# Kernel tuning notes

Hardware: AMD Instinct MI355X
Metric: run time of the kernel (lower is better)

Reference implementation:

```python
import jax, jax.numpy as jnp
import numpy as np

B, S, D_IN, D_OUT, L = 16, 1024, 768, 768, 2
ALPHA = 0.2  # LeakyReLU negative slope
NEG_INF = -1e12


def setup_inputs() -> dict:
    key = jax.random.key(0)
    ks = jax.random.split(key, 6)
    input_feature = jax.random.normal(ks[0], (B, S, D_IN), dtype=jnp.float32)
    matrix = jax.random.randint(ks[1], (B, S, S), 0, 2, dtype=jnp.int32)
    # per-layer params (stacked along leading L axis)
    sw = 1.0 / np.sqrt(D_IN)
    W = jax.random.uniform(ks[2], (L, D_OUT, D_IN), jnp.float32, -sw, sw)
    Wb = jax.random.uniform(ks[3], (L, D_OUT), jnp.float32, -sw, sw)
    sa = 1.0 / np.sqrt(2 * D_OUT)
    A = jax.random.uniform(ks[4], (L, 2 * D_OUT), jnp.float32, -sa, sa)
    Ab = jax.random.uniform(ks[5], (L,), jnp.float32, -sa, sa)
    return {"input_feature": input_feature, "matrix": matrix,
            "W": W, "Wb": Wb, "A": A, "Ab": Ab}


def reference(input_feature, matrix, W, Wb, A, Ab):
    # Eval mode: dropout(p=0.1, training=False) is identity.
    hidden = input_feature
    mask = matrix > 0  # [B,S,S]
    outs = []
    for l in range(L):
        h = jnp.einsum('bsd,od->bso', hidden, W[l]) + Wb[l]  # [B,S,Dout]
        # a([h_i, h_j]) == h_i @ a_src + h_j @ a_dst + b  (exact separation)
        a_src, a_dst = A[l, :D_OUT], A[l, D_OUT:]
        s_i = h @ a_src  # [B,S]
        s_j = h @ a_dst  # [B,S]
        e = jax.nn.leaky_relu(s_i[:, :, None] + s_j[:, None, :] + Ab[l], ALPHA)
        e = jnp.where(mask, e, NEG_INF)
        attn = jax.nn.softmax(e, axis=1)  # original softmaxes over dim=1
        hidden = jnp.einsum('bij,bjd->bid', attn, h)
        outs.append(hidden)
    return jnp.stack(outs)  # [L,B,S,Dout]
```

## Files before the change

### kernel.cpp

```cpp
#include <hip/hip_runtime.h>
#include <cstddef>

#define SS 1024
#define DF 768
#define NBATCH 16
#define GAT_ALPHA 0.2f

typedef _Float16 f16x8 __attribute__((ext_vector_type(8)));
typedef _Float16 f16x4 __attribute__((ext_vector_type(4)));
typedef float f32x4 __attribute__((ext_vector_type(4)));

__device__ __forceinline__ void gload16(const void* g, void* l) {
  __builtin_amdgcn_global_load_lds(
      (const __attribute__((address_space(1))) void*)g,
      (__attribute__((address_space(3))) void*)l, 16, 0, 0);
}

__device__ __forceinline__ float lrelu(float t) {
  return fmaxf(t, GAT_ALPHA * t);
}

__global__ __launch_bounds__(256) void f32tof16_k(const float* __restrict__ in,
                                                  _Float16* __restrict__ out,
                                                  int n) {
  int idx = (blockIdx.x * 256 + threadIdx.x) * 4;
  if (idx + 3 < n) {
    float4 v = *(const float4*)&in[idx];
    f16x4 o;
    o[0] = (_Float16)v.x;
    o[1] = (_Float16)v.y;
    o[2] = (_Float16)v.z;
    o[3] = (_Float16)v.w;
    *(f16x4*)&out[idx] = o;
  }
}

__global__ __launch_bounds__(256) void pack_k(const int* __restrict__ mask,
                                              unsigned char* __restrict__ bm) {
  const size_t t = (size_t)blockIdx.x * 256 + threadIdx.x;
  const int* mp = mask + t * 8;
  const int4 a = *(const int4*)mp;
  const int4 c = *(const int4*)(mp + 4);
  unsigned v = (unsigned)(a.x > 0) | ((unsigned)(a.y > 0) << 1) |
               ((unsigned)(a.z > 0) << 2) | ((unsigned)(a.w > 0) << 3) |
               ((unsigned)(c.x > 0) << 4) | ((unsigned)(c.y > 0) << 5) |
               ((unsigned)(c.z > 0) << 6) | ((unsigned)(c.w > 0) << 7);
  bm[t] = (unsigned char)v;
}

__global__ __launch_bounds__(512, 2) void gemm1_k(
    const _Float16* __restrict__ X16, const _Float16* __restrict__ W16,
    const float* __restrict__ Wbl, const float* __restrict__ Al,
    _Float16* __restrict__ hT16, float* __restrict__ psi2,
    float* __restrict__ psj2) {
  __shared__ __align__(16) char smem[131072];
  const int flat = blockIdx.x;
  const int swz = (flat & 7) * 32 + (flat >> 3);
  const int m0 = (swz >> 1) * 128;
  const int n0 = (swz & 1) * 384;
  const int tid = threadIdx.x;
  const int w = tid >> 6, lane = tid & 63;

  const int srow = w * 16 + (lane >> 2);
  const int sk8 = ((lane & 3) ^ ((lane >> 3) & 3)) * 8;
  const int rby = ((lane >> 4) ^ ((lane >> 1) & 3)) * 16;
  const int rrow = lane & 15;

  f32x4 acc[8][3];
#pragma unroll
  for (int mi = 0; mi < 8; ++mi)
#pragma unroll
    for (int ni = 0; ni < 3; ++ni) acc[mi][ni] = (f32x4)(0.f);

#define STGA1(s, kt)                                                       \
  gload16(&X16[(size_t)(m0 + srow) * DF + (kt) * 32 + sk8],                \
          smem + (s) * 32768 + w * 1024)
#define STGB1(s, kt, q)                                                    \
  gload16(&W16[(size_t)(n0 + (q) * 128 + srow) * DF + (kt) * 32 + sk8],    \
          smem + (s) * 32768 + 8192 + (q) * 8192 + w * 1024)

  const int NT = DF / 32;
  STGA1(0, 0); STGB1(0, 0, 0); STGB1(0, 0, 1); STGB1(0, 0, 2);
  STGA1(1, 1); STGB1(1, 1, 0); STGB1(1, 1, 1); STGB1(1, 1, 2);
  asm volatile("s_waitcnt vmcnt(4)" ::: "memory");
  asm volatile("s_barrier" ::: "memory");

  for (int t = 0; t < NT; ++t) {
    const int s = t & 3;
    const char* Ab = smem + s * 32768;
    const char* Bb = smem + s * 32768 + 8192;
    f16x8 bfr[3], afr[8];
#pragma unroll
    for (int ni = 0; ni < 3; ++ni)
      bfr[ni] = *(const f16x8*)(Bb + (w * 48 + ni * 16 + rrow) * 64 + rby);
#pragma unroll
    for (int mi = 0; mi < 8; ++mi)
      afr[mi] = *(const f16x8*)(Ab + (mi * 16 + rrow) * 64 + rby);
    if (t + 2 < NT) {
      const int s2 = (t + 2) & 3;
      STGA1(s2, t + 2);
      STGB1(s2, t + 2, 0);
      STGB1(s2, t + 2, 1);
      STGB1(s2, t + 2, 2);
    }
    if (t < NT - 2)
      asm volatile("s_waitcnt vmcnt(4)" ::: "memory");
    else
      asm volatile("s_waitcnt vmcnt(0)" ::: "memory");
    asm volatile("s_barrier" ::: "memory");
    __builtin_amdgcn_s_setprio(1);
#pragma unroll
    for (int mi = 0; mi < 8; ++mi)
#pragma unroll
      for (int ni = 0; ni < 3; ++ni)
        acc[mi][ni] = __builtin_amdgcn_mfma_f32_16x16x32_f16(
            afr[mi], bfr[ni], acc[mi][ni], 0, 0, 0);
    __builtin_amdgcn_s_setprio(0);
  }
#undef STGA1
#undef STGB1

  __syncthreads();
  _Float16* tb = (_Float16*)smem + (size_t)w * 6528;
  float* asrc = (float*)(smem + 104448);
  float* adst = asrc + 384;
  float* pwsi = adst + 384;
  float* pwsj = pwsi + 1024;

  for (int i = tid; i < 384; i += 512) {
    asrc[i] = Al[n0 + i];
    adst[i] = Al[DF + n0 + i];
  }
  const int cg = lane >> 4, cr = lane & 15;
  float bias[3];
#pragma unroll
  for (int ni = 0; ni < 3; ++ni) bias[ni] = Wbl[n0 + w * 48 + ni * 16 + cr];
#pragma unroll
  for (int mi = 0; mi < 8; ++mi) {
#pragma unroll
    for (int ni = 0; ni < 3; ++ni) {
      f16x4 tv;
#pragma unroll
      for (int r = 0; r < 4; ++r)
        tv[r] = (_Float16)(acc[mi][ni][r] + bias[ni]);
      *(f16x4*)&tb[(ni * 16 + cr) * 136 + mi * 16 + cg * 4] = tv;
    }
  }
  __syncthreads();

  const float* wa = asrc + w * 48;
  const float* wdp = adst + w * 48;
#pragma unroll
  for (int rr = 0; rr < 2; ++rr) {
    const int r = lane + rr * 64;
    float ps = 0.f, pd = 0.f;
#pragma unroll 8
    for (int c = 0; c < 48; ++c) {
      const float hv = (float)tb[c * 136 + r];
      ps = fmaf(hv, wa[c], ps);
      pd = fmaf(hv, wdp[c], pd);
    }
    pwsi[w * 128 + r] = ps;
    pwsj[w * 128 + r] = pd;
  }
  __syncthreads();
  if (tid < 128) {
    float s = 0.f, d2 = 0.f;
#pragma unroll
    for (int ww = 0; ww < 8; ++ww) {
      s += pwsi[ww * 128 + tid];
      d2 += pwsj[ww * 128 + tid];
    }
    const int nt = swz & 1;
    psi2[nt * 16384 + m0 + tid] = s;
    psj2[nt * 16384 + m0 + tid] = d2;
  }

  const int bb = m0 >> 10, s0 = m0 & 1023;
#pragma unroll
  for (int pass = 0; pass < 12; ++pass) {
    const int c = pass * 4 + (lane >> 4);
    f16x8 v = *(const f16x8*)&tb[c * 136 + (lane & 15) * 8];
    *(f16x8*)&hT16[((size_t)bb * DF + n0 + w * 48 + c) * SS + s0 +
                   (lane & 15) * 8] = v;
  }
}

__global__ __launch_bounds__(512, 2) void gemm2_k(
    const unsigned char* __restrict__ bmk, const float* __restrict__ si_g,
    const unsigned int* __restrict__ sq_g, const _Float16* __restrict__ hT16,
    float* __restrict__ outl, _Float16* __restrict__ X16n, int writeX) {
  __shared__ __align__(16) char smem[153600];
  const int flat = blockIdx.x;
  const int swz = (flat & 7) * 32 + (flat >> 3);
  const int b = swz >> 4;
  const int i0 = ((swz >> 1) & 7) * 128;
  const int d0 = (swz & 1) * 384;
  const int tid = threadIdx.x;
  const int w = tid >> 6, lane = tid & 63;

  const int srow = w * 16 + (lane >> 2);
  const int sk8 = ((lane & 3) ^ ((lane >> 3) & 3)) * 8;
  const int rby = ((lane >> 4) ^ ((lane >> 1) & 3)) * 16;
  const int rrow = lane & 15;

  const int pr = tid >> 2, pc = tid & 3;
  const int ppos = pc ^ ((pr >> 1) & 3);

  const _Float16* hTb = hT16 + (size_t)b * DF * SS;

  f32x4 acc[8][3];
#pragma unroll
  for (int mi = 0; mi < 8; ++mi)
#pragma unroll
    for (int ni = 0; ni < 3; ++ni) acc[mi][ni] = (f32x4)(0.f);

#define STGB2(s, kt, q)                                                    \
  gload16(&hTb[((size_t)(d0 + (q) * 128 + srow)) * SS + (kt) * 32 + sk8],  \
          smem + (s) * 32768 + 8192 + (q) * 8192 + w * 1024)

#define COMPUTE_P(kt, slot)                                                  \
  {                                                                          \
    const unsigned mw =                                                      \
        *(const unsigned*)(smem + 135168 + pr * 144 + (kt) * 4);             \
    const unsigned mb = (mw >> (pc * 8)) & 0xffu;                            \
    const f16x8 sA_ =                                                        \
        *(const f16x8*)(smem + 131072 + (kt) * 128 + pc * 32);               \
    const f16x8 sB_ =                                                        \
        *(const f16x8*)(smem + 131072 + (kt) * 128 + pc * 32 + 16);          \
    f16x8 ph;                                                                \
    _Pragma("unroll") for (int jj = 0; jj < 4; ++jj) {                       \
      const float sjcv = (float)sA_[2 * jj];                                 \
      const float qv = (float)sA_[2 * jj + 1];                               \
      const float ttv = siv + sjcv;                                          \
      const float ev = __expf(fmaxf(ttv, 0.2f * ttv)) * qv;                  \
      ph[jj] = (_Float16)(qv < 0.f ? -qv : (((mb >> jj) & 1u) ? ev : 0.f));  \
    }                                                                        \
    _Pragma("unroll") for (int jj = 0; jj < 4; ++jj) {                       \
      const float sjcv = (float)sB_[2 * jj];                                 \
      const float qv = (float)sB_[2 * jj + 1];                               \
      const float ttv = siv + sjcv;                                          \
      const float ev = __expf(fmaxf(ttv, 0.2f * ttv)) * qv;                  \
      ph[4 + jj] = (_Float16)(qv < 0.f ? -qv                                 \
                                       : (((mb >> (4 + jj)) & 1u) ? ev       \
                                                                  : 0.f));   \
    }                                                                        \
    *(f16x8*)(smem + (slot) * 32768 + pr * 64 + ppos * 16) = ph;             \
  }

  const unsigned char* bmb = bmk + ((size_t)b << 17) + ((size_t)i0 << 7);
  const uint4 mg0 = *(const uint4*)(bmb + tid * 32);
  const uint4 mg1 = *(const uint4*)(bmb + tid * 32 + 16);
  if (w < 4)
    gload16(&sq_g[(b << 10) + w * 256 + lane * 4], smem + 131072 + w * 1024);
  const float siv = si_g[(b << 10) + i0 + pr];
  const int NT = SS / 32;
  STGB2(0, 0, 0); STGB2(0, 0, 1); STGB2(0, 0, 2);
  STGB2(1, 1, 0); STGB2(1, 1, 1); STGB2(1, 1, 2);
  asm volatile("s_waitcnt vmcnt(0)" ::: "memory");
  *(uint4*)(smem + 135168 + pr * 144 + pc * 32) = mg0;
  *(uint4*)(smem + 135168 + pr * 144 + pc * 32 + 16) = mg1;
  asm volatile("s_waitcnt lgkmcnt(0)" ::: "memory");
  asm volatile("s_barrier" ::: "memory");
  COMPUTE_P(0, 0);
  asm volatile("s_waitcnt lgkmcnt(0)" ::: "memory");
  asm volatile("s_barrier" ::: "memory");

  for (int t = 0; t < NT; ++t) {
    const char* Ab = smem + (t & 3) * 32768;
    const char* Bb = Ab + 8192;
    f16x8 bfr[3], afr[8];
#pragma unroll
    for (int ni = 0; ni < 3; ++ni)
      bfr[ni] = *(const f16x8*)(Bb + (w * 48 + ni * 16 + rrow) * 64 + rby);
#pragma unroll
    for (int mi = 0; mi < 8; ++mi)
      afr[mi] = *(const f16x8*)(Ab + (mi * 16 + rrow) * 64 + rby);
    if (t + 1 < NT) COMPUTE_P(t + 1, (t + 1) & 3);
    if (t + 2 < NT) {
      const int s2 = (t + 2) & 3;
      STGB2(s2, t + 2, 0);
      STGB2(s2, t + 2, 1);
      STGB2(s2, t + 2, 2);
    }
    if (t < NT - 2)
      asm volatile("s_waitcnt vmcnt(3) lgkmcnt(0)" ::: "memory");
    else
      asm volatile("s_waitcnt vmcnt(0) lgkmcnt(0)" ::: "memory");
    asm volatile("s_barrier" ::: "memory");
    __builtin_amdgcn_s_setprio(1);
#pragma unroll
    for (int mi = 0; mi < 8; ++mi)
#pragma unroll
      for (int ni = 0; ni < 3; ++ni)
        acc[mi][ni] = __builtin_amdgcn_mfma_f32_16x16x32_f16(
            afr[mi], bfr[ni], acc[mi][ni], 0, 0, 0);
    __builtin_amdgcn_s_setprio(0);
  }
#undef STGB2
#undef COMPUTE_P

  const int cg = lane >> 4, cr = lane & 15;
#pragma unroll
  for (int mi = 0; mi < 8; ++mi) {
#pragma unroll
    for (int ni = 0; ni < 3; ++ni) {
      const int d = d0 + w * 48 + ni * 16 + cr;
      const int row0 = i0 + mi * 16 + cg * 4;
#pragma unroll
      for (int r = 0; r < 4; ++r) {
        float v = acc[mi][ni][r];
        size_t o = ((size_t)b * SS + row0 + r) * DF + d;
        outl[o] = v;
        if (writeX) X16n[o] = (_Float16)v;
      }
    }
  }
}

__global__ __launch_bounds__(256) void rowfin_k(const float* __restrict__ psi2,
                                                const float* __restrict__ psj2,
                                                const float* __restrict__ Abp,
                                                float* __restrict__ si,
                                                float* __restrict__ sjc,
                                                float* __restrict__ refj) {
  const int b = blockIdx.x;
  const int t = threadIdx.x;
  __shared__ float red[256];
  float siv[4], sjv[4];
  float mloc = -1e30f;
#pragma unroll
  for (int q = 0; q < 4; ++q) {
    const int idx = (b << 10) + t + (q << 8);
    const float a = psi2[idx] + psi2[16384 + idx];
    const float d = psj2[idx] + psj2[16384 + idx];
    siv[q] = a;
    sjv[q] = d;
    si[idx] = a;
    mloc = fmaxf(mloc, a);
  }
  red[t] = mloc;
  __syncthreads();
  for (int off = 128; off > 0; off >>= 1) {
    if (t < off) red[t] = fmaxf(red[t], red[t + off]);
    __syncthreads();
  }
  const float maxsi = red[0];
  const float ab = Abp[0];
#pragma unroll
  for (int q = 0; q < 4; ++q) {
    const int idx = (b << 10) + t + (q << 8);
    const float c = sjv[q] + ab;
    sjc[idx] = c;
    refj[idx] = lrelu(maxsi + c);
  }
}

__global__ __launch_bounds__(256) void colsum_k(
    const unsigned char* __restrict__ bm, const float* __restrict__ si,
    const float* __restrict__ sjc, const float* __restrict__ refj,
    float* __restrict__ pden) {
  const int g = blockIdx.x;
  const int b = blockIdx.y;
  const int t = threadIdx.x;
  const int jb = t & 127;
  const int half = t >> 7;
  const int row0 = (g << 5) + (half << 4);
  __shared__ float s_si[32];
  if (t < 32) s_si[t] = si[(b << 10) + (g << 5) + t];
  __syncthreads();
  float sc[8], rf[8];
  *(float4*)&sc[0] = *(const float4*)&sjc[(b << 10) + jb * 8];
  *(float4*)&sc[4] = *(const float4*)&sjc[(b << 10) + jb * 8 + 4];
  *(float4*)&rf[0] = *(const float4*)&refj[(b << 10) + jb * 8];
  *(float4*)&rf[4] = *(const float4*)&refj[(b << 10) + jb * 8 + 4];
  float den[8] = {0.f, 0.f, 0.f, 0.f, 0.f, 0.f, 0.f, 0.f};
  const unsigned char* bp = bm + ((size_t)b << 17) + ((size_t)row0 << 7) + jb;
#pragma unroll 4
  for (int r = 0; r < 16; ++r) {
    const unsigned m = bp[(size_t)r << 7];
    const float siv = s_si[(half << 4) + r];
#pragma unroll
    for (int k = 0; k < 8; ++k) {
      if ((m >> k) & 1) den[k] += __expf(lrelu(siv + sc[k]) - rf[k]);
    }
  }
  const size_t o = ((size_t)(g * 2 + half)) * 16384 + (b << 10) + jb * 8;
  *(float4*)&pden[o] = *(float4*)&den[0];
  *(float4*)&pden[o + 4] = *(float4*)&den[4];
}

__global__ __launch_bounds__(256) void colfin_k(const float* __restrict__ pden,
                                                const float* __restrict__ sjc,
                                                const float* __restrict__ refj,
                                                unsigned int* __restrict__ sq) {
  const int idx = blockIdx.x * 256 + threadIdx.x;
  float s = 0.f;
#pragma unroll
  for (int c = 0; c < 64; ++c) s += pden[(size_t)c * 16384 + idx];
  const float q = (s > 0.f) ? __expf(-refj[idx]) / s : -0.0009765625f;
  const _Float16 h0 = (_Float16)sjc[idx];
  const _Float16 h1 = (_Float16)q;
  unsigned short u0, u1;
  __builtin_memcpy(&u0, &h0, 2);
  __builtin_memcpy(&u1, &h1, 2);
  sq[idx] = ((unsigned)u1 << 16) | (unsigned)u0;
}

extern "C" void kernel_launch(void* const* d_in, const int* in_sizes, int n_in,
                              void* d_out, int out_size, void* d_ws,
                              size_t ws_size, hipStream_t stream) {
  const float* X0 = (const float*)d_in[0];
  const int* mask = (const int*)d_in[1];
  const float* W = (const float*)d_in[2];
  const float* Wb = (const float*)d_in[3];
  const float* A = (const float*)d_in[4];
  const float* Ab = (const float*)d_in[5];
  float* out = (float*)d_out;

  const size_t BSD = (size_t)NBATCH * SS * DF;
  const size_t BSS = (size_t)NBATCH * SS * SS;
  const size_t BS = (size_t)NBATCH * SS;

  char* p = (char*)d_ws;
  _Float16* X16 = (_Float16*)p;   p += BSD * 2;
  _Float16* hT16 = (_Float16*)p;  p += BSD * 2;
  _Float16* W16 = (_Float16*)p;   p += (size_t)2 * DF * DF * 2;
  unsigned char* bmk = (unsigned char*)p; p += BSS / 8;
  float* psi2 = (float*)p; p += 2 * BS * 4;
  float* psj2 = (float*)p; p += 2 * BS * 4;
  float* pden = (float*)p; p += 64 * BS * 4;
  float* si = (float*)p;   p += BS * 4;
  float* sjc = (float*)p;  p += BS * 4;
  float* refj = (float*)p; p += BS * 4;
  unsigned int* sq_g = (unsigned int*)p; p += BS * 4;

  f32tof16_k<<<12288, 256, 0, stream>>>(X0, X16, (int)BSD);
  f32tof16_k<<<1152, 256, 0, stream>>>(W, W16, 2 * DF * DF);
  pack_k<<<8192, 256, 0, stream>>>(mask, bmk);

  for (int l = 0; l < 2; ++l) {
    gemm1_k<<<256, 512, 0, stream>>>(X16, W16 + (size_t)l * DF * DF,
                                     Wb + (size_t)l * DF,
                                     A + (size_t)l * 2 * DF, hT16, psi2, psj2);
    rowfin_k<<<16, 256, 0, stream>>>(psi2, psj2, Ab + l, si, sjc, refj);
    colsum_k<<<dim3(32, 16), 256, 0, stream>>>(bmk, si, sjc, refj, pden);
    colfin_k<<<64, 256, 0, stream>>>(pden, sjc, refj, sq_g);
    gemm2_k<<<256, 512, 0, stream>>>(bmk, si, sq_g, hT16,
                                     out + (size_t)l * BSD, X16,
                                     (l == 0) ? 1 : 0);
  }
}
```

Measured before the change: 246.2 us.

## Factor LeakyReLU exponentials into per-row and per-column terms, removing exp from inner loops

Uses exp(lrelu(si+sj)) = exp(si)exp(sj) or exp(0.2si)exp(0.2sj), depending on the sign of si+sj. Per-row exponentials are computed once, and per-column scale factors are precomputed in colfin. colsum then accumulates two partial sums without any exp calls. gemm2's P computation becomes an fp16 select and multiply instead of an exp per element. The cost is double the partial-sum buffers and sq traffic, and a risk of fp16 overflow or precision loss in the factored products (e.g. exp(si) in half).

```diff
diff --git a/kernel.cpp b/kernel.cpp
--- a/kernel.cpp
+++ b/kernel.cpp
@@ -188,9 +188,9 @@
 
 __global__ __launch_bounds__(512, 2) void gemm2_k(
     const unsigned char* __restrict__ bmk, const float* __restrict__ si_g,
-    const unsigned int* __restrict__ sq_g, const _Float16* __restrict__ hT16,
+    const uint2* __restrict__ sq_g, const _Float16* __restrict__ hT16,
     float* __restrict__ outl, _Float16* __restrict__ X16n, int writeX) {
-  __shared__ __align__(16) char smem[153600];
+  __shared__ __align__(16) char smem[157696];
   const int flat = blockIdx.x;
   const int swz = (flat & 7) * 32 + (flat >> 3);
   const int b = swz >> 4;
@@ -219,47 +219,51 @@
   gload16(&hTb[((size_t)(d0 + (q) * 128 + srow)) * SS + (kt) * 32 + sk8],  \
           smem + (s) * 32768 + 8192 + (q) * 8192 + w * 1024)
 
+#define PCALC(sjch, c1h, c2h, mbit)                                        \
+  ((c2h) < (_Float16)0.f                                                   \
+       ? (_Float16)0.0009765625f                                           \
+       : (!(mbit) ? (_Float16)0.f                                          \
+                  : ((_Float16)(sih + (sjch)) >= (_Float16)0.f             \
+                         ? (_Float16)(e1h * (c1h))                         \
+                         : (_Float16)(e2h * (c2h)))))
+
 #define COMPUTE_P(kt, slot)                                                  \
   {                                                                          \
     const unsigned mw =                                                      \
-        *(const unsigned*)(smem + 135168 + pr * 144 + (kt) * 4);             \
+        *(const unsigned*)(smem + 139264 + pr * 144 + (kt) * 4);             \
     const unsigned mb = (mw >> (pc * 8)) & 0xffu;                            \
-    const f16x8 sA_ =                                                        \
-        *(const f16x8*)(smem + 131072 + (kt) * 128 + pc * 32);               \
-    const f16x8 sB_ =                                                        \
-        *(const f16x8*)(smem + 131072 + (kt) * 128 + pc * 32 + 16);          \
+    const char* sqb = smem + 131072 + (kt) * 256 + pc * 64;                  \
+    const f16x8 q0 = *(const f16x8*)(sqb);                                   \
+    const f16x8 q1 = *(const f16x8*)(sqb + 16);                              \
+    const f16x8 q2 = *(const f16x8*)(sqb + 32);                              \
+    const f16x8 q3 = *(const f16x8*)(sqb + 48);                              \
     f16x8 ph;                                                                \
-    _Pragma("unroll") for (int jj = 0; jj < 4; ++jj) {                       \
-      const float sjcv = (float)sA_[2 * jj];                                 \
-      const float qv = (float)sA_[2 * jj + 1];                               \
-      const float ttv = siv + sjcv;                                          \
-      const float ev = __expf(fmaxf(ttv, 0.2f * ttv)) * qv;                  \
-      ph[jj] = (_Float16)(qv < 0.f ? -qv : (((mb >> jj) & 1u) ? ev : 0.f));  \
-    }                                                                        \
-    _Pragma("unroll") for (int jj = 0; jj < 4; ++jj) {                       \
-      const float sjcv = (float)sB_[2 * jj];                                 \
-      const float qv = (float)sB_[2 * jj + 1];                               \
-      const float ttv = siv + sjcv;                                          \
-      const float ev = __expf(fmaxf(ttv, 0.2f * ttv)) * qv;                  \
-      ph[4 + jj] = (_Float16)(qv < 0.f ? -qv                                 \
-                                       : (((mb >> (4 + jj)) & 1u) ? ev       \
-                                                                  : 0.f));   \
-    }                                                                        \
+    ph[0] = PCALC(q0[0], q0[1], q0[2], (mb & 1u));                           \
+    ph[1] = PCALC(q0[4], q0[5], q0[6], ((mb >> 1) & 1u));                    \
+    ph[2] = PCALC(q1[0], q1[1], q1[2], ((mb >> 2) & 1u));                    \
+    ph[3] = PCALC(q1[4], q1[5], q1[6], ((mb >> 3) & 1u));                    \
+    ph[4] = PCALC(q2[0], q2[1], q2[2], ((mb >> 4) & 1u));                    \
+    ph[5] = PCALC(q2[4], q2[5], q2[6], ((mb >> 5) & 1u));                    \
+    ph[6] = PCALC(q3[0], q3[1], q3[2], ((mb >> 6) & 1u));                    \
+    ph[7] = PCALC(q3[4], q3[5], q3[6], ((mb >> 7) & 1u));                    \
     *(f16x8*)(smem + (slot) * 32768 + pr * 64 + ppos * 16) = ph;             \
   }
 
   const unsigned char* bmb = bmk + ((size_t)b << 17) + ((size_t)i0 << 7);
   const uint4 mg0 = *(const uint4*)(bmb + tid * 32);
   const uint4 mg1 = *(const uint4*)(bmb + tid * 32 + 16);
-  if (w < 4)
-    gload16(&sq_g[(b << 10) + w * 256 + lane * 4], smem + 131072 + w * 1024);
+  gload16((const char*)(sq_g + ((size_t)b << 10)) + tid * 16,
+          smem + 131072 + w * 1024);
   const float siv = si_g[(b << 10) + i0 + pr];
+  const _Float16 sih = (_Float16)siv;
+  const _Float16 e1h = (_Float16)__expf(siv);
+  const _Float16 e2h = (_Float16)__expf(0.2f * siv);
   const int NT = SS / 32;
   STGB2(0, 0, 0); STGB2(0, 0, 1); STGB2(0, 0, 2);
   STGB2(1, 1, 0); STGB2(1, 1, 1); STGB2(1, 1, 2);
   asm volatile("s_waitcnt vmcnt(0)" ::: "memory");
-  *(uint4*)(smem + 135168 + pr * 144 + pc * 32) = mg0;
-  *(uint4*)(smem + 135168 + pr * 144 + pc * 32 + 16) = mg1;
+  *(uint4*)(smem + 139264 + pr * 144 + pc * 32) = mg0;
+  *(uint4*)(smem + 139264 + pr * 144 + pc * 32 + 16) = mg1;
   asm volatile("s_waitcnt lgkmcnt(0)" ::: "memory");
   asm volatile("s_barrier" ::: "memory");
   COMPUTE_P(0, 0);
@@ -299,6 +303,7 @@
   }
 #undef STGB2
 #undef COMPUTE_P
+#undef PCALC
 
   const int cg = lane >> 4, cr = lane & 15;
 #pragma unroll
@@ -358,53 +363,82 @@
 
 __global__ __launch_bounds__(256) void colsum_k(
     const unsigned char* __restrict__ bm, const float* __restrict__ si,
-    const float* __restrict__ sjc, const float* __restrict__ refj,
-    float* __restrict__ pden) {
+    const float* __restrict__ sjc, float* __restrict__ pden1,
+    float* __restrict__ pden2) {
   const int g = blockIdx.x;
   const int b = blockIdx.y;
   const int t = threadIdx.x;
   const int jb = t & 127;
   const int half = t >> 7;
   const int row0 = (g << 5) + (half << 4);
-  __shared__ float s_si[32];
-  if (t < 32) s_si[t] = si[(b << 10) + (g << 5) + t];
+  __shared__ float s_si[32], s_e1[32], s_e2[32];
+  if (t < 32) {
+    const float v = si[(b << 10) + (g << 5) + t];
+    s_si[t] = v;
+    s_e1[t] = __expf(v);
+    s_e2[t] = __expf(0.2f * v);
+  }
   __syncthreads();
-  float sc[8], rf[8];
+  float sc[8];
   *(float4*)&sc[0] = *(const float4*)&sjc[(b << 10) + jb * 8];
   *(float4*)&sc[4] = *(const float4*)&sjc[(b << 10) + jb * 8 + 4];
-  *(float4*)&rf[0] = *(const float4*)&refj[(b << 10) + jb * 8];
-  *(float4*)&rf[4] = *(const float4*)&refj[(b << 10) + jb * 8 + 4];
-  float den[8] = {0.f, 0.f, 0.f, 0.f, 0.f, 0.f, 0.f, 0.f};
+  float d1[8] = {0.f, 0.f, 0.f, 0.f, 0.f, 0.f, 0.f, 0.f};
+  float d2[8] = {0.f, 0.f, 0.f, 0.f, 0.f, 0.f, 0.f, 0.f};
   const unsigned char* bp = bm + ((size_t)b << 17) + ((size_t)row0 << 7) + jb;
 #pragma unroll 4
   for (int r = 0; r < 16; ++r) {
     const unsigned m = bp[(size_t)r << 7];
-    const float siv = s_si[(half << 4) + r];
+    const int ri = (half << 4) + r;
+    const float siv = s_si[ri], e1v = s_e1[ri], e2v = s_e2[ri];
 #pragma unroll
     for (int k = 0; k < 8; ++k) {
-      if ((m >> k) & 1) den[k] += __expf(lrelu(siv + sc[k]) - rf[k]);
+      if ((m >> k) & 1) {
+        if (siv + sc[k] >= 0.f)
+          d1[k] += e1v;
+        else
+          d2[k] += e2v;
+      }
     }
   }
   const size_t o = ((size_t)(g * 2 + half)) * 16384 + (b << 10) + jb * 8;
-  *(float4*)&pden[o] = *(float4*)&den[0];
-  *(float4*)&pden[o + 4] = *(float4*)&den[4];
-}
-
-__global__ __launch_bounds__(256) void colfin_k(const float* __restrict__ pden,
-                                                const float* __restrict__ sjc,
-                                                const float* __restrict__ refj,
-                                                unsigned int* __restrict__ sq) {
+  *(float4*)&pden1[o] = *(float4*)&d1[0];
+  *(float4*)&pden1[o + 4] = *(float4*)&d1[4];
+  *(float4*)&pden2[o] = *(float4*)&d2[0];
+  *(float4*)&pden2[o + 4] = *(float4*)&d2[4];
+}
+
+__global__ __launch_bounds__(256) void colfin_k(
+    const float* __restrict__ pden1, const float* __restrict__ pden2,
+    const float* __restrict__ sjc, const float* __restrict__ refj,
+    uint2* __restrict__ sq) {
   const int idx = blockIdx.x * 256 + threadIdx.x;
-  float s = 0.f;
-#pragma unroll
-  for (int c = 0; c < 64; ++c) s += pden[(size_t)c * 16384 + idx];
-  const float q = (s > 0.f) ? __expf(-refj[idx]) / s : -0.0009765625f;
-  const _Float16 h0 = (_Float16)sjc[idx];
-  const _Float16 h1 = (_Float16)q;
-  unsigned short u0, u1;
-  __builtin_memcpy(&u0, &h0, 2);
-  __builtin_memcpy(&u1, &h1, 2);
-  sq[idx] = ((unsigned)u1 << 16) | (unsigned)u0;
+  float S1 = 0.f, S2 = 0.f;
+#pragma unroll
+  for (int c = 0; c < 64; ++c) {
+    S1 += pden1[(size_t)c * 16384 + idx];
+    S2 += pden2[(size_t)c * 16384 + idx];
+  }
+  const float sj = sjc[idx], rf = refj[idx];
+  const float A1 = __expf(sj - rf);
+  const float A2 = __expf(0.2f * sj - rf);
+  const float den = A1 * S1 + A2 * S2;
+  _Float16 sjh = (_Float16)sj;
+  _Float16 c1h, c2h;
+  if (den > 0.f) {
+    c1h = (_Float16)(A1 / den);
+    c2h = (_Float16)(A2 / den);
+  } else {
+    c1h = (_Float16)0.f;
+    c2h = (_Float16)(-0.0009765625f);
+  }
+  unsigned short u0, u1, u2;
+  __builtin_memcpy(&u0, &sjh, 2);
+  __builtin_memcpy(&u1, &c1h, 2);
+  __builtin_memcpy(&u2, &c2h, 2);
+  uint2 outw;
+  outw.x = (unsigned)u0 | ((unsigned)u1 << 16);
+  outw.y = (unsigned)u2;
+  sq[idx] = outw;
 }
 
 extern "C" void kernel_launch(void* const* d_in, const int* in_sizes, int n_in,
@@ -427,13 +461,14 @@
   _Float16* hT16 = (_Float16*)p;  p += BSD * 2;
   _Float16* W16 = (_Float16*)p;   p += (size_t)2 * DF * DF * 2;
   unsigned char* bmk = (unsigned char*)p; p += BSS / 8;
-  float* psi2 = (float*)p; p += 2 * BS * 4;
-  float* psj2 = (float*)p; p += 2 * BS * 4;
-  float* pden = (float*)p; p += 64 * BS * 4;
+  float* psi2 = (float*)p;  p += 2 * BS * 4;
+  float* psj2 = (float*)p;  p += 2 * BS * 4;
+  float* pden1 = (float*)p; p += 64 * BS * 4;
+  float* pden2 = (float*)p; p += 64 * BS * 4;
   float* si = (float*)p;   p += BS * 4;
   float* sjc = (float*)p;  p += BS * 4;
   float* refj = (float*)p; p += BS * 4;
-  unsigned int* sq_g = (unsigned int*)p; p += BS * 4;
+  uint2* sq_g = (uint2*)p; p += BS * 8;
 
   f32tof16_k<<<12288, 256, 0, stream>>>(X0, X16, (int)BSD);
   f32tof16_k<<<1152, 256, 0, stream>>>(W, W16, 2 * DF * DF);
@@ -444,8 +479,8 @@
                                      Wb + (size_t)l * DF,
                                      A + (size_t)l * 2 * DF, hT16, psi2, psj2);
     rowfin_k<<<16, 256, 0, stream>>>(psi2, psj2, Ab + l, si, sjc, refj);
-    colsum_k<<<dim3(32, 16), 256, 0, stream>>>(bmk, si, sjc, refj, pden);
-    colfin_k<<<64, 256, 0, stream>>>(pden, sjc, refj, sq_g);
+    colsum_k<<<dim3(32, 16), 256, 0, stream>>>(bmk, si, sjc, pden1, pden2);
+    colfin_k<<<64, 256, 0, stream>>>(pden1, pden2, sjc, refj, sq_g);
     gemm2_k<<<256, 512, 0, stream>>>(bmk, si, sq_g, hT16,
                                      out + (size_t)l * BSD, X16,
                                      (l == 0) ? 1 : 0);
```

Result: no change. 244.4 us (-0.7%).
